# Performance work log

Hardware: AMD Instinct MI355X
Metric: run time of the kernel (lower is better)

Reference implementation:

```python
import math
import jax, jax.numpy as jnp
import numpy as np

HIDDEN = 2880
HEAD_DIM = 64
N_HEADS = 64
N_KV = 8
Q_MULT = N_HEADS // N_KV  # 8
QKV_DIM = HEAD_DIM * (N_HEADS + 2 * N_KV)  # 5120
SLIDING_WINDOW = 128
SM_SCALE = 1.0 / math.sqrt(HEAD_DIM)
ROPE_BASE = 150000.0
ROPE_SCALING = 32.0
INIT_CTX = 4096
NTK_ALPHA = 1.0
NTK_BETA = 32.0
EPS = 1e-5
N_TOKENS = 1536


def rope_tables(n):
    # YaRN-style inv_freq mixing (scaling_factor > 1 branch)
    d = HEAD_DIM
    freq = ROPE_BASE ** (jnp.arange(0, d, 2, dtype=jnp.float32) / d)
    concentration = 0.1 * math.log(ROPE_SCALING) + 1.0
    d_half = d / 2
    low = d_half * math.log(INIT_CTX / (NTK_BETA * 2 * math.pi)) / math.log(ROPE_BASE)
    high = d_half * math.log(INIT_CTX / (NTK_ALPHA * 2 * math.pi)) / math.log(ROPE_BASE)
    interpolation = 1.0 / (ROPE_SCALING * freq)
    extrapolation = 1.0 / freq
    ramp = (jnp.arange(d_half, dtype=jnp.float32) - low) / (high - low)
    mask = 1.0 - jnp.clip(ramp, 0.0, 1.0)
    inv_freq = interpolation * (1.0 - mask) + extrapolation * mask
    t = jnp.arange(n, dtype=jnp.float32)
    freqs = t[:, None] * inv_freq[None, :]  # (n, d/2)
    return jnp.cos(freqs) * concentration, jnp.sin(freqs) * concentration


def apply_rotary(x, cos, sin):
    # x: (n, H, d); cos/sin: (n, d/2)
    c = cos[:, None, :]
    s = sin[:, None, :]
    x1, x2 = jnp.split(x, 2, axis=-1)
    return jnp.concatenate([x1 * c - x2 * s, x2 * c + x1 * s], axis=-1)


def setup_inputs() -> dict:
    key = jax.random.key(0)
    ks = jax.random.split(key, 7)
    x = jax.random.normal(ks[0], (N_TOKENS, HIDDEN), dtype=jnp.float32)
    norm_scale = jnp.ones((HIDDEN,), dtype=jnp.float32)
    qkv_w = jax.random.normal(ks[1], (QKV_DIM, HIDDEN), dtype=jnp.float32) * 0.02
    qkv_b = jax.random.normal(ks[2], (QKV_DIM,), dtype=jnp.float32) * 0.02
    out_w = jax.random.normal(ks[3], (HIDDEN, HEAD_DIM * N_HEADS), dtype=jnp.float32) * 0.02
    out_b = jax.random.normal(ks[4], (HIDDEN,), dtype=jnp.float32) * 0.02
    sinks = jax.random.normal(ks[5], (N_HEADS,), dtype=jnp.float32)
    return {"x": x, "norm_scale": norm_scale, "qkv_w": qkv_w, "qkv_b": qkv_b,
            "out_w": out_w, "out_b": out_b, "sinks": sinks}


def reference(x, norm_scale, qkv_w, qkv_b, out_w, out_b, sinks):
    n = x.shape[0]
    # RMSNorm (fp32)
    t = x * jax.lax.rsqrt(jnp.mean(x * x, axis=-1, keepdims=True) + EPS) * norm_scale
    # fused QKV projection
    qkv = t @ qkv_w.T + qkv_b  # (n, QKV_DIM)
    q = qkv[:, : N_HEADS * HEAD_DIM].reshape(n, N_KV, Q_MULT, HEAD_DIM)
    k = qkv[:, N_HEADS * HEAD_DIM : (N_HEADS + N_KV) * HEAD_DIM].reshape(n, N_KV, HEAD_DIM)
    v = qkv[:, (N_HEADS + N_KV) * HEAD_DIM :].reshape(n, N_KV, HEAD_DIM)
    # RoPE
    cos, sin = rope_tables(n)
    q = apply_rotary(q.reshape(n, N_HEADS, HEAD_DIM), cos, sin).reshape(n, N_KV, Q_MULT, HEAD_DIM)
    k = apply_rotary(k, cos, sin)
    # attention with causal + sliding-window mask and sink logits
    i = jnp.arange(n)[:, None]
    j = jnp.arange(n)[None, :]
    allowed = (j <= i) & (j > i - SLIDING_WINDOW)
    mask = jnp.where(allowed, 0.0, -jnp.inf).astype(jnp.float32)  # (q, k)
    scores = jnp.einsum('qhmd,khd->hmqk', q, k) * SM_SCALE + mask[None, None, :, :]
    s = sinks.reshape(N_KV, Q_MULT, 1, 1)
    s = jnp.broadcast_to(s, (N_KV, Q_MULT, n, 1))
    logits = jnp.concatenate([scores, s], axis=-1)
    w = jax.nn.softmax(logits, axis=-1)[..., :-1]  # drop sink column
    attn = jnp.einsum('hmqk,khd->qhmd', w, v).reshape(n, N_HEADS * HEAD_DIM)
    # output projection + residual
    return x + attn @ out_w.T + out_b
```

## Files before the change

### kernel.cpp

```cpp
#include <hip/hip_runtime.h>

typedef __attribute__((ext_vector_type(8))) short bf16x8;
typedef __attribute__((ext_vector_type(4))) float f32x4;

#define HIDDEN 2880
#define QKV_DIM 5120
#define NH 64
#define NKV 8
#define HD 64
#define ATT_DIM 4096
#define WINDOW 128
#define SM_SCALE 0.125f

__device__ __forceinline__ ushort f2bf(float f) {
  union { float f; unsigned u; } a; a.f = f;
  unsigned r = a.u + 0x7fffu + ((a.u >> 16) & 1u);
  return (ushort)(r >> 16);
}
__device__ __forceinline__ float bf2f(ushort u) {
  union { unsigned u; float f; } a; a.u = ((unsigned)u) << 16;
  return a.f;
}

__device__ __forceinline__ void gload_lds16(const void* g, void* l) {
  __builtin_amdgcn_global_load_lds((const __attribute__((address_space(1))) void*)g,
                                   (__attribute__((address_space(3))) void*)l, 16, 0, 0);
}

__global__ __launch_bounds__(256) void cvt_f32_bf16(const float* __restrict__ in,
                                                    ushort* __restrict__ out, int n4) {
  int i = blockIdx.x * blockDim.x + threadIdx.x;
  int stride = gridDim.x * blockDim.x;
  for (; i < n4; i += stride) {
    float4 v = ((const float4*)in)[i];
    ushort4 o = { f2bf(v.x), f2bf(v.y), f2bf(v.z), f2bf(v.w) };
    ((ushort4*)out)[i] = o;
  }
}

__global__ __launch_bounds__(256) void rmsnorm_bf16(const float* __restrict__ x,
                                                    const float* __restrict__ scale,
                                                    ushort* __restrict__ t) {
  int row = blockIdx.x;
  int tid = threadIdx.x;
  const float4* xr = (const float4*)(x + (size_t)row * HIDDEN);
  float4 a0 = xr[tid];
  float4 a1 = xr[tid + 256];
  bool has2 = tid < 208;
  float4 a2 = has2 ? xr[tid + 512] : float4{0.f, 0.f, 0.f, 0.f};
  float ss = a0.x*a0.x + a0.y*a0.y + a0.z*a0.z + a0.w*a0.w
           + a1.x*a1.x + a1.y*a1.y + a1.z*a1.z + a1.w*a1.w
           + a2.x*a2.x + a2.y*a2.y + a2.z*a2.z + a2.w*a2.w;
  for (int m = 1; m < 64; m <<= 1) ss += __shfl_xor(ss, m, 64);
  __shared__ float red[4];
  if ((tid & 63) == 0) red[tid >> 6] = ss;
  __syncthreads();
  ss = red[0] + red[1] + red[2] + red[3];
  float r = rsqrtf(ss / (float)HIDDEN + 1e-5f);
  ushort4* tr = (ushort4*)(t + (size_t)row * HIDDEN);
  const float4* sc4 = (const float4*)scale;
  {
    float4 s = sc4[tid];
    ushort4 o = { f2bf(a0.x*r*s.x), f2bf(a0.y*r*s.y), f2bf(a0.z*r*s.z), f2bf(a0.w*r*s.w) };
    tr[tid] = o;
  }
  {
    float4 s = sc4[tid + 256];
    ushort4 o = { f2bf(a1.x*r*s.x), f2bf(a1.y*r*s.y), f2bf(a1.z*r*s.z), f2bf(a1.w*r*s.w) };
    tr[tid + 256] = o;
  }
  if (has2) {
    float4 s = sc4[tid + 512];
    ushort4 o = { f2bf(a2.x*r*s.x), f2bf(a2.y*r*s.y), f2bf(a2.z*r*s.z), f2bf(a2.w*r*s.w) };
    tr[tid + 512] = o;
  }
}

template <int MASK_N>
__global__ __launch_bounds__(512)
void gemm_8p(const ushort* __restrict__ A, const ushort* __restrict__ B,
             ushort* __restrict__ P, int M, int N, int K, int NSK) {
  __shared__ __align__(16) ushort Al[2][256 * 64];
  __shared__ __align__(16) ushort Bl[2][256 * 64];
  const int tid = threadIdx.x;
  const int wave = tid >> 6, lane = tid & 63;
  const int l15 = lane & 15, hi = lane >> 4;

  int nwg = gridDim.x, orig = blockIdx.x;
  int q8 = nwg >> 3, r8 = nwg & 7, xcd = orig & 7, seq = orig >> 3;
  int swz = (xcd < r8 ? xcd * (q8 + 1) : r8 * (q8 + 1) + (xcd - r8) * q8) + seq;
  int nm = M >> 8;
  int bm = swz % nm, bn = swz / nm;
  const int row0 = bm * 256, col0 = bn * 256;
  const int sk = blockIdx.y;
  const int NTtot = K >> 6;
  const int tt0 = sk * NTtot / NSK, tt1 = (sk + 1) * NTtot / NSK;
  ushort* Pp = P + (size_t)sk * M * N;

  const int wrow = (wave >> 2) * 128;
  const int wcol = (wave & 3) * 64;
  const int srow = lane >> 3;
  const int schunk = (lane & 7) ^ srow;

  f32x4 acc[8][4] = {};

  auto stageA = [&](int t, int r) {
    int row = row0 + r * 64 + wave * 8 + srow;
    gload_lds16(A + (size_t)row * K + (t << 6) + schunk * 8,
                &Al[t & 1][(r * 64 + wave * 8) * 64]);
  };
  auto stageB = [&](int t, int r) {
    int brow = col0 + r * 64 + wave * 8 + srow;
    if (MASK_N) { if (brow > N - 1) brow = N - 1; }
    gload_lds16(B + (size_t)brow * K + (t << 6) + schunk * 8,
                &Bl[t & 1][(r * 64 + wave * 8) * 64]);
  };
  auto stageAll = [&](int t) {
#pragma unroll
    for (int r = 0; r < 4; ++r) { stageA(t, r); stageB(t, r); }
  };
  auto LDA = [&](bf16x8 (&dst)[4][2], int mh, const char* base) {
#pragma unroll
    for (int mt = 0; mt < 4; ++mt)
#pragma unroll
      for (int ks = 0; ks < 2; ++ks) {
        int rr = wrow + mh * 64 + mt * 16 + l15;
        int off = (rr * 128 + ks * 64 + hi * 16) ^ ((rr & 7) << 4);
        dst[mt][ks] = *(const bf16x8*)(base + off);
      }
  };
  auto LDB = [&](bf16x8 (&dst)[2][2], int nh, const char* base) {
#pragma unroll
    for (int nt = 0; nt < 2; ++nt)
#pragma unroll
      for (int ks = 0; ks < 2; ++ks) {
        int rr = wcol + nh * 32 + nt * 16 + l15;
        int off = (rr * 128 + ks * 64 + hi * 16) ^ ((rr & 7) << 4);
        dst[nt][ks] = *(const bf16x8*)(base + off);
      }
  };
  auto MMA = [&](bf16x8 (&a)[4][2], bf16x8 (&b)[2][2], int mh, int nh) {
    __builtin_amdgcn_s_setprio(1);
#pragma unroll
    for (int ks = 0; ks < 2; ++ks)
#pragma unroll
      for (int nt = 0; nt < 2; ++nt)
#pragma unroll
        for (int mt = 0; mt < 4; ++mt)
          acc[mh * 4 + mt][nh * 2 + nt] = __builtin_amdgcn_mfma_f32_16x16x32_bf16(
              a[mt][ks], b[nt][ks], acc[mh * 4 + mt][nh * 2 + nt], 0, 0, 0);
    __builtin_amdgcn_s_setprio(0);
  };

  stageAll(tt0);
  bool two = (tt1 - tt0 > 1);
  if (two) {
    stageAll(tt0 + 1);
    asm volatile("s_waitcnt vmcnt(8)" ::: "memory");
  } else {
    asm volatile("s_waitcnt vmcnt(0)" ::: "memory");
  }
  __builtin_amdgcn_s_barrier();

  for (int t = tt0; t < tt1; ++t) {
    const char* Ab = (const char*)&Al[t & 1][0];
    const char* Bb = (const char*)&Bl[t & 1][0];
    bool pre = (t + 2 < tt1);
    bf16x8 afr[4][2], bf0[2][2], bf1[2][2];
    LDA(afr, 0, Ab);
    LDB(bf0, 0, Bb);
    __builtin_amdgcn_s_barrier();
    MMA(afr, bf0, 0, 0);
    __builtin_amdgcn_s_barrier();
    LDB(bf1, 1, Bb);
    if (pre) { stageA(t + 2, 0); stageA(t + 2, 2); }
    __builtin_amdgcn_s_barrier();
    MMA(afr, bf1, 0, 1);
    __builtin_amdgcn_s_barrier();
    LDA(afr, 1, Ab);
    if (pre) { stageB(t + 2, 0); stageB(t + 2, 1); stageB(t + 2, 2); stageB(t + 2, 3); }
    __builtin_amdgcn_s_barrier();
    MMA(afr, bf1, 1, 1);
    __builtin_amdgcn_s_barrier();
    if (pre) { stageA(t + 2, 1); stageA(t + 2, 3); }
    __builtin_amdgcn_s_barrier();
    MMA(afr, bf0, 1, 0);
    if (pre) asm volatile("s_waitcnt vmcnt(8)" ::: "memory");
    else     asm volatile("s_waitcnt vmcnt(0)" ::: "memory");
    __builtin_amdgcn_s_barrier();
  }

#pragma unroll
  for (int mtg = 0; mtg < 8; ++mtg) {
#pragma unroll
    for (int nt = 0; nt < 4; ++nt) {
#pragma unroll
      for (int rr = 0; rr < 4; ++rr) {
        int row = row0 + wrow + mtg * 16 + (hi << 2) + rr;
        int col = col0 + wcol + nt * 16 + l15;
        if (!MASK_N || col < N) Pp[(size_t)row * N + col] = f2bf(acc[mtg][nt][rr]);
      }
    }
  }
}

__global__ __launch_bounds__(256)
void reduce_out(const float* __restrict__ x, const float* __restrict__ b,
                const ushort* __restrict__ p, int nsk, size_t stride,
                float* __restrict__ out, int n4, int N) {
  int i = blockIdx.x * blockDim.x + threadIdx.x;
  if (i >= n4) return;
  float4 v = ((const float4*)x)[i];
  int col = (i * 4) % N;
  float4 bb = *(const float4*)(b + col);
  v.x += bb.x; v.y += bb.y; v.z += bb.z; v.w += bb.w;
  for (int s = 0; s < nsk; ++s) {
    ushort4 pv = *(const ushort4*)(p + s * stride + (size_t)i * 4);
    v.x += bf2f(pv.x); v.y += bf2f(pv.y); v.z += bf2f(pv.z); v.w += bf2f(pv.w);
  }
  ((float4*)out)[i] = v;
}

__global__ __launch_bounds__(256)
void rope_split(const ushort* __restrict__ p, size_t stride, const float* __restrict__ qkvb,
                ushort* __restrict__ qb, ushort* __restrict__ kb, ushort* __restrict__ vb) {
  int tok = blockIdx.x;
  int tid = threadIdx.x;
  __shared__ float cs[32], sn[32];
  if (tid < 32) {
    float d = (float)tid;
    float freq = powf(150000.0f, d / 32.0f);
    float conc = 0.1f * logf(32.0f) + 1.0f;
    float lg = logf(150000.0f);
    float low = 32.0f * logf(4096.0f / (32.0f * 6.2831853f)) / lg;
    float high = 32.0f * logf(4096.0f / 6.2831853f) / lg;
    float ramp = (d - low) / (high - low);
    float cl = fminf(fmaxf(ramp, 0.0f), 1.0f);
    float mask = 1.0f - cl;
    float inv_freq = (1.0f - mask) / (32.0f * freq) + mask / freq;
    float fr = (float)tok * inv_freq;
    cs[tid] = cosf(fr) * conc;
    sn[tid] = sinf(fr) * conc;
  }
  __syncthreads();
  const ushort* r0 = p + (size_t)tok * QKV_DIM;
  const ushort* r1 = r0 + stride;
  auto ld = [&](int c) { return bf2f(r0[c]) + bf2f(r1[c]) + qkvb[c]; };
#pragma unroll
  for (int it = 0; it < 8; ++it) {
    int pp = tid + it * 256;
    int hd = pp >> 5, d = pp & 31;
    float x1 = ld(hd * 64 + d), x2 = ld(hd * 64 + d + 32);
    float c = cs[d], s = sn[d];
    size_t o = ((size_t)tok * NH + hd) * HD + d;
    qb[o] = f2bf(x1 * c - x2 * s);
    qb[o + 32] = f2bf(x2 * c + x1 * s);
  }
  {
    int pp = tid;
    int hd = pp >> 5, d = pp & 31;
    float x1 = ld(4096 + hd * 64 + d), x2 = ld(4096 + hd * 64 + d + 32);
    float c = cs[d], s = sn[d];
    size_t o = ((size_t)tok * NKV + hd) * HD + d;
    kb[o] = f2bf(x1 * c - x2 * s);
    kb[o + 32] = f2bf(x2 * c + x1 * s);
  }
#pragma unroll
  for (int it = 0; it < 2; ++it) {
    int pp = tid + it * 256;
    vb[(size_t)tok * (NKV * HD) + pp] = f2bf(ld(4608 + pp));
  }
}

__global__ __launch_bounds__(512)
void attn_cvt(const ushort* __restrict__ qb, const ushort* __restrict__ kb,
              const ushort* __restrict__ vb, const float* __restrict__ sinks,
              ushort* __restrict__ attn, int n, int nattn,
              const float* __restrict__ w, ushort* __restrict__ wout, int n4w) {
  __shared__ __align__(16) ushort Kl[160 * 64];
  __shared__ __align__(16) ushort Vt[64 * 168];
  __shared__ __align__(16) ushort Pl[8][16 * 40];
  int tid = threadIdx.x;
  if ((int)blockIdx.x >= nattn) {
    int i = ((int)blockIdx.x - nattn) * 512 + tid;
    int stride = (gridDim.x - nattn) * 512;
    for (; i < n4w; i += stride) {
      float4 v = ((const float4*)w)[i];
      ushort4 o = { f2bf(v.x), f2bf(v.y), f2bf(v.z), f2bf(v.w) };
      ((ushort4*)wout)[i] = o;
    }
    return;
  }
  int wave = tid >> 6, lane = tid & 63;
  int l15 = lane & 15, hi = lane >> 4;
  int qstart = ((int)blockIdx.x >> 3) * 16;
  int kv = (int)blockIdx.x & 7;
  int head = kv * 8 + wave;
  int key0 = qstart - 128;

  for (int i = 0; i < 3; ++i) {
    int rowb = i * 64 + wave * 8;
    if (rowb < 160) {
      int r = rowb + (lane >> 3);
      int gj = key0 + r; if (gj < 0) gj = 0;
      int chunk = (lane & 7) ^ (lane >> 3);
      gload_lds16(kb + ((size_t)gj * NKV + kv) * HD + chunk * 8, Kl + rowb * 64);
    }
  }
  for (int e = tid; e < 160 * 16; e += 512) {
    int j = e >> 4, d4 = (e & 15) << 2;
    int gj = key0 + j; if (gj < 0) gj = 0;
    ushort4 v = *(const ushort4*)(vb + ((size_t)gj * NKV + kv) * HD + d4);
    Vt[(d4 + 0) * 168 + j] = v.x;
    Vt[(d4 + 1) * 168 + j] = v.y;
    Vt[(d4 + 2) * 168 + j] = v.z;
    Vt[(d4 + 3) * 168 + j] = v.w;
  }
  bf16x8 qf[2];
#pragma unroll
  for (int ks = 0; ks < 2; ++ks) {
    int r = qstart + l15;
    int kk = ks * 32 + hi * 8;
    qf[ks] = *(const bf16x8*)(qb + ((size_t)r * NH + head) * HD + kk);
  }
  __syncthreads();

  f32x4 s[10] = {};
#pragma unroll
  for (int nt = 0; nt < 10; ++nt) {
#pragma unroll
    for (int ks = 0; ks < 2; ++ks) {
      int r = nt * 16 + l15;
      int off = (r * 128 + (ks * 32 + hi * 8) * 2) ^ ((r & 7) << 4);
      bf16x8 kf = *(const bf16x8*)((const char*)Kl + off);
      s[nt] = __builtin_amdgcn_mfma_f32_16x16x32_bf16(qf[ks], kf, s[nt], 0, 0, 0);
    }
  }

  float lrow[4];
  float snk = sinks[head];
#pragma unroll
  for (int r = 0; r < 4; ++r) {
    int i = qstart + hi * 4 + r;
    float mx = -1e30f;
#pragma unroll
    for (int nt = 0; nt < 10; ++nt) {
      int j = key0 + nt * 16 + l15;
      bool ok = (j >= 0) && (j <= i) && (j > i - WINDOW);
      float val = ok ? s[nt][r] * SM_SCALE : -1e30f;
      s[nt][r] = val;
      mx = fmaxf(mx, val);
    }
    mx = fmaxf(mx, __shfl_xor(mx, 1, 64));
    mx = fmaxf(mx, __shfl_xor(mx, 2, 64));
    mx = fmaxf(mx, __shfl_xor(mx, 4, 64));
    mx = fmaxf(mx, __shfl_xor(mx, 8, 64));
    mx = fmaxf(mx, snk);
    float sum = 0.f;
#pragma unroll
    for (int nt = 0; nt < 10; ++nt) {
      float pv = __expf(s[nt][r] - mx);
      s[nt][r] = pv;
      sum += pv;
    }
    sum += __shfl_xor(sum, 1, 64);
    sum += __shfl_xor(sum, 2, 64);
    sum += __shfl_xor(sum, 4, 64);
    sum += __shfl_xor(sum, 8, 64);
    sum += __expf(snk - mx);
    lrow[r] = sum;
  }

  f32x4 o[4] = {};
#pragma unroll
  for (int kc = 0; kc < 5; ++kc) {
#pragma unroll
    for (int t2 = 0; t2 < 2; ++t2) {
      int nt = kc * 2 + t2;
#pragma unroll
      for (int r = 0; r < 4; ++r)
        Pl[wave][(hi * 4 + r) * 40 + t2 * 16 + l15] = f2bf(s[nt][r]);
    }
    bf16x8 pa = *(const bf16x8*)(&Pl[wave][l15 * 40 + hi * 8]);
#pragma unroll
    for (int nt = 0; nt < 4; ++nt) {
      int d = nt * 16 + l15;
      int kk = kc * 32 + hi * 8;
      bf16x8 vf = *(const bf16x8*)(&Vt[d * 168 + kk]);
      o[nt] = __builtin_amdgcn_mfma_f32_16x16x32_bf16(pa, vf, o[nt], 0, 0, 0);
    }
  }

#pragma unroll
  for (int nt = 0; nt < 4; ++nt)
#pragma unroll
    for (int r = 0; r < 4; ++r) {
      int row = qstart + hi * 4 + r;
      int d = nt * 16 + l15;
      float val = o[nt][r] / lrow[r];
      attn[((size_t)row * NH + head) * HD + d] = f2bf(val);
    }
}

extern "C" void kernel_launch(void* const* d_in, const int* in_sizes, int n_in,
                              void* d_out, int out_size, void* d_ws, size_t ws_size,
                              hipStream_t stream) {
  const float* x      = (const float*)d_in[0];
  const float* nscale = (const float*)d_in[1];
  const float* qkv_w  = (const float*)d_in[2];
  const float* qkv_b  = (const float*)d_in[3];
  const float* out_w  = (const float*)d_in[4];
  const float* out_b  = (const float*)d_in[5];
  const float* sinks  = (const float*)d_in[6];
  float* out = (float*)d_out;
  int n = in_sizes[0] / HIDDEN;

  char* ws = (char*)d_ws;
  size_t off = 0;
  auto alloc = [&](size_t bytes) {
    char* p = ws + off;
    off += (bytes + 255) & ~(size_t)255;
    return p;
  };
  ushort* t_bf    = (ushort*)alloc((size_t)n * HIDDEN * 2);
  ushort* qkvw_bf = (ushort*)alloc((size_t)QKV_DIM * HIDDEN * 2);
  ushort* outw_bf = (ushort*)alloc((size_t)HIDDEN * ATT_DIM * 2);
  ushort* q_bf    = (ushort*)alloc((size_t)n * NH * HD * 2);
  ushort* k_bf    = (ushort*)alloc((size_t)n * NKV * HD * 2);
  ushort* v_bf    = (ushort*)alloc((size_t)n * NKV * HD * 2);
  ushort* attn    = (ushort*)alloc((size_t)n * ATT_DIM * 2);
  size_t qkv_ps = (size_t)n * QKV_DIM;
  size_t out_ps = (size_t)n * HIDDEN;
  size_t pelems = 2 * qkv_ps > 3 * out_ps ? 2 * qkv_ps : 3 * out_ps;
  ushort* partials = (ushort*)alloc(pelems * 2);

  cvt_f32_bf16<<<1024, 256, 0, stream>>>(qkv_w, qkvw_bf, QKV_DIM * HIDDEN / 4);
  rmsnorm_bf16<<<n, 256, 0, stream>>>(x, nscale, t_bf);
  gemm_8p<0><<<dim3((n / 256) * (QKV_DIM / 256), 2), 512, 0, stream>>>(
      t_bf, qkvw_bf, partials, n, QKV_DIM, HIDDEN, 2);
  rope_split<<<n, 256, 0, stream>>>(partials, qkv_ps, qkv_b, q_bf, k_bf, v_bf);
  int nattn = (n / 16) * NKV;
  attn_cvt<<<nattn + 320, 512, 0, stream>>>(q_bf, k_bf, v_bf, sinks, attn, n, nattn,
                                            out_w, outw_bf, HIDDEN * ATT_DIM / 4);
  gemm_8p<1><<<dim3((n / 256) * 12, 3), 512, 0, stream>>>(
      attn, outw_bf, partials, n, HIDDEN, ATT_DIM, 3);
  reduce_out<<<(n * HIDDEN / 4 + 255) / 256, 256, 0, stream>>>(
      x, out_b, partials, 3, out_ps, out, n * HIDDEN / 4, HIDDEN);
}
```

Before: 168.6 us.

## Shrink GEMM tiles to 128x128, drop QKV split-K, fuse bias and norm/convert kernels

```diff
diff --git a/kernel.cpp b/kernel.cpp
--- a/kernel.cpp
+++ b/kernel.cpp
@@ -27,22 +27,22 @@
                                    (__attribute__((address_space(3))) void*)l, 16, 0, 0);
 }
 
-__global__ __launch_bounds__(256) void cvt_f32_bf16(const float* __restrict__ in,
-                                                    ushort* __restrict__ out, int n4) {
-  int i = blockIdx.x * blockDim.x + threadIdx.x;
-  int stride = gridDim.x * blockDim.x;
-  for (; i < n4; i += stride) {
-    float4 v = ((const float4*)in)[i];
-    ushort4 o = { f2bf(v.x), f2bf(v.y), f2bf(v.z), f2bf(v.w) };
-    ((ushort4*)out)[i] = o;
-  }
-}
-
-__global__ __launch_bounds__(256) void rmsnorm_bf16(const float* __restrict__ x,
-                                                    const float* __restrict__ scale,
-                                                    ushort* __restrict__ t) {
+__global__ __launch_bounds__(256)
+void norm_cvt(const float* __restrict__ x, const float* __restrict__ scale,
+              ushort* __restrict__ t, int n,
+              const float* __restrict__ w, ushort* __restrict__ wout, int n4w) {
+  int tid = threadIdx.x;
+  if ((int)blockIdx.x >= n) {
+    int i = ((int)blockIdx.x - n) * 256 + tid;
+    int stride = (gridDim.x - n) * 256;
+    for (; i < n4w; i += stride) {
+      float4 v = ((const float4*)w)[i];
+      ushort4 o = { f2bf(v.x), f2bf(v.y), f2bf(v.z), f2bf(v.w) };
+      ((ushort4*)wout)[i] = o;
+    }
+    return;
+  }
   int row = blockIdx.x;
-  int tid = threadIdx.x;
   const float4* xr = (const float4*)(x + (size_t)row * HIDDEN);
   float4 a0 = xr[tid];
   float4 a1 = xr[tid + 256];
@@ -76,12 +76,13 @@
   }
 }
 
-template <int MASK_N>
-__global__ __launch_bounds__(512)
-void gemm_8p(const ushort* __restrict__ A, const ushort* __restrict__ B,
-             ushort* __restrict__ P, int M, int N, int K, int NSK) {
-  __shared__ __align__(16) ushort Al[2][256 * 64];
-  __shared__ __align__(16) ushort Bl[2][256 * 64];
+template <int MASK_N, int FUSE_BIAS>
+__global__ __launch_bounds__(256)
+void gemm_128(const ushort* __restrict__ A, const ushort* __restrict__ B,
+              const float* __restrict__ bias, ushort* __restrict__ P,
+              int M, int N, int K, int NSK) {
+  __shared__ __align__(16) ushort Al[2][128 * 64];
+  __shared__ __align__(16) ushort Bl[2][128 * 64];
   const int tid = threadIdx.x;
   const int wave = tid >> 6, lane = tid & 63;
   const int l15 = lane & 15, hi = lane >> 4;
@@ -89,42 +90,43 @@
   int nwg = gridDim.x, orig = blockIdx.x;
   int q8 = nwg >> 3, r8 = nwg & 7, xcd = orig & 7, seq = orig >> 3;
   int swz = (xcd < r8 ? xcd * (q8 + 1) : r8 * (q8 + 1) + (xcd - r8) * q8) + seq;
-  int nm = M >> 8;
+  int nm = M >> 7;
   int bm = swz % nm, bn = swz / nm;
-  const int row0 = bm * 256, col0 = bn * 256;
+  const int row0 = bm * 128, col0 = bn * 128;
   const int sk = blockIdx.y;
   const int NTtot = K >> 6;
   const int tt0 = sk * NTtot / NSK, tt1 = (sk + 1) * NTtot / NSK;
   ushort* Pp = P + (size_t)sk * M * N;
 
-  const int wrow = (wave >> 2) * 128;
-  const int wcol = (wave & 3) * 64;
+  const int wrow = (wave >> 1) * 64;
+  const int wcol = (wave & 1) * 64;
   const int srow = lane >> 3;
   const int schunk = (lane & 7) ^ srow;
 
-  f32x4 acc[8][4] = {};
+  f32x4 acc[4][4] = {};
 
   auto stageA = [&](int t, int r) {
-    int row = row0 + r * 64 + wave * 8 + srow;
-    gload_lds16(A + (size_t)row * K + (t << 6) + schunk * 8,
-                &Al[t & 1][(r * 64 + wave * 8) * 64]);
+    int rowb = r * 32 + wave * 8;
+    gload_lds16(A + (size_t)(row0 + rowb + srow) * K + (t << 6) + schunk * 8,
+                &Al[t & 1][rowb * 64]);
   };
   auto stageB = [&](int t, int r) {
-    int brow = col0 + r * 64 + wave * 8 + srow;
+    int rowb = r * 32 + wave * 8;
+    int brow = col0 + rowb + srow;
     if (MASK_N) { if (brow > N - 1) brow = N - 1; }
     gload_lds16(B + (size_t)brow * K + (t << 6) + schunk * 8,
-                &Bl[t & 1][(r * 64 + wave * 8) * 64]);
+                &Bl[t & 1][rowb * 64]);
   };
   auto stageAll = [&](int t) {
 #pragma unroll
     for (int r = 0; r < 4; ++r) { stageA(t, r); stageB(t, r); }
   };
-  auto LDA = [&](bf16x8 (&dst)[4][2], int mh, const char* base) {
-#pragma unroll
-    for (int mt = 0; mt < 4; ++mt)
+  auto LDA = [&](bf16x8 (&dst)[2][2], int mh, const char* base) {
+#pragma unroll
+    for (int mt = 0; mt < 2; ++mt)
 #pragma unroll
       for (int ks = 0; ks < 2; ++ks) {
-        int rr = wrow + mh * 64 + mt * 16 + l15;
+        int rr = wrow + (mh * 2 + mt) * 16 + l15;
         int off = (rr * 128 + ks * 64 + hi * 16) ^ ((rr & 7) << 4);
         dst[mt][ks] = *(const bf16x8*)(base + off);
       }
@@ -134,21 +136,21 @@
     for (int nt = 0; nt < 2; ++nt)
 #pragma unroll
       for (int ks = 0; ks < 2; ++ks) {
-        int rr = wcol + nh * 32 + nt * 16 + l15;
+        int rr = wcol + (nh * 2 + nt) * 16 + l15;
         int off = (rr * 128 + ks * 64 + hi * 16) ^ ((rr & 7) << 4);
         dst[nt][ks] = *(const bf16x8*)(base + off);
       }
   };
-  auto MMA = [&](bf16x8 (&a)[4][2], bf16x8 (&b)[2][2], int mh, int nh) {
+  auto MMA = [&](bf16x8 (&a)[2][2], bf16x8 (&b)[2][2], int mh, int nh) {
     __builtin_amdgcn_s_setprio(1);
 #pragma unroll
     for (int ks = 0; ks < 2; ++ks)
 #pragma unroll
       for (int nt = 0; nt < 2; ++nt)
 #pragma unroll
-        for (int mt = 0; mt < 4; ++mt)
-          acc[mh * 4 + mt][nh * 2 + nt] = __builtin_amdgcn_mfma_f32_16x16x32_bf16(
-              a[mt][ks], b[nt][ks], acc[mh * 4 + mt][nh * 2 + nt], 0, 0, 0);
+        for (int mt = 0; mt < 2; ++mt)
+          acc[mh * 2 + mt][nh * 2 + nt] = __builtin_amdgcn_mfma_f32_16x16x32_bf16(
+              a[mt][ks], b[nt][ks], acc[mh * 2 + mt][nh * 2 + nt], 0, 0, 0);
     __builtin_amdgcn_s_setprio(0);
   };
 
@@ -166,7 +168,7 @@
     const char* Ab = (const char*)&Al[t & 1][0];
     const char* Bb = (const char*)&Bl[t & 1][0];
     bool pre = (t + 2 < tt1);
-    bf16x8 afr[4][2], bf0[2][2], bf1[2][2];
+    bf16x8 afr[2][2], bf0[2][2], bf1[2][2];
     LDA(afr, 0, Ab);
     LDB(bf0, 0, Bb);
     __builtin_amdgcn_s_barrier();
@@ -191,14 +193,18 @@
   }
 
 #pragma unroll
-  for (int mtg = 0; mtg < 8; ++mtg) {
+  for (int mt = 0; mt < 4; ++mt) {
 #pragma unroll
     for (int nt = 0; nt < 4; ++nt) {
 #pragma unroll
       for (int rr = 0; rr < 4; ++rr) {
-        int row = row0 + wrow + mtg * 16 + (hi << 2) + rr;
+        int row = row0 + wrow + mt * 16 + (hi << 2) + rr;
         int col = col0 + wcol + nt * 16 + l15;
-        if (!MASK_N || col < N) Pp[(size_t)row * N + col] = f2bf(acc[mtg][nt][rr]);
+        if (!MASK_N || col < N) {
+          float v = acc[mt][nt][rr];
+          if (FUSE_BIAS) v += bias[col];
+          Pp[(size_t)row * N + col] = f2bf(v);
+        }
       }
     }
   }
@@ -222,7 +228,7 @@
 }
 
 __global__ __launch_bounds__(256)
-void rope_split(const ushort* __restrict__ p, size_t stride, const float* __restrict__ qkvb,
+void rope_split(const ushort* __restrict__ qkv,
                 ushort* __restrict__ qb, ushort* __restrict__ kb, ushort* __restrict__ vb) {
   int tok = blockIdx.x;
   int tid = threadIdx.x;
@@ -243,14 +249,12 @@
     sn[tid] = sinf(fr) * conc;
   }
   __syncthreads();
-  const ushort* r0 = p + (size_t)tok * QKV_DIM;
-  const ushort* r1 = r0 + stride;
-  auto ld = [&](int c) { return bf2f(r0[c]) + bf2f(r1[c]) + qkvb[c]; };
+  const ushort* row = qkv + (size_t)tok * QKV_DIM;
 #pragma unroll
   for (int it = 0; it < 8; ++it) {
     int pp = tid + it * 256;
     int hd = pp >> 5, d = pp & 31;
-    float x1 = ld(hd * 64 + d), x2 = ld(hd * 64 + d + 32);
+    float x1 = bf2f(row[hd * 64 + d]), x2 = bf2f(row[hd * 64 + d + 32]);
     float c = cs[d], s = sn[d];
     size_t o = ((size_t)tok * NH + hd) * HD + d;
     qb[o] = f2bf(x1 * c - x2 * s);
@@ -259,7 +263,7 @@
   {
     int pp = tid;
     int hd = pp >> 5, d = pp & 31;
-    float x1 = ld(4096 + hd * 64 + d), x2 = ld(4096 + hd * 64 + d + 32);
+    float x1 = bf2f(row[4096 + hd * 64 + d]), x2 = bf2f(row[4096 + hd * 64 + d + 32]);
     float c = cs[d], s = sn[d];
     size_t o = ((size_t)tok * NKV + hd) * HD + d;
     kb[o] = f2bf(x1 * c - x2 * s);
@@ -268,7 +272,7 @@
 #pragma unroll
   for (int it = 0; it < 2; ++it) {
     int pp = tid + it * 256;
-    vb[(size_t)tok * (NKV * HD) + pp] = f2bf(ld(4608 + pp));
+    vb[(size_t)tok * (NKV * HD) + pp] = row[4608 + pp];
   }
 }
 
@@ -425,25 +429,24 @@
   ushort* t_bf    = (ushort*)alloc((size_t)n * HIDDEN * 2);
   ushort* qkvw_bf = (ushort*)alloc((size_t)QKV_DIM * HIDDEN * 2);
   ushort* outw_bf = (ushort*)alloc((size_t)HIDDEN * ATT_DIM * 2);
+  ushort* qkv_bf  = (ushort*)alloc((size_t)n * QKV_DIM * 2);
   ushort* q_bf    = (ushort*)alloc((size_t)n * NH * HD * 2);
   ushort* k_bf    = (ushort*)alloc((size_t)n * NKV * HD * 2);
   ushort* v_bf    = (ushort*)alloc((size_t)n * NKV * HD * 2);
   ushort* attn    = (ushort*)alloc((size_t)n * ATT_DIM * 2);
-  size_t qkv_ps = (size_t)n * QKV_DIM;
   size_t out_ps = (size_t)n * HIDDEN;
-  size_t pelems = 2 * qkv_ps > 3 * out_ps ? 2 * qkv_ps : 3 * out_ps;
-  ushort* partials = (ushort*)alloc(pelems * 2);
-
-  cvt_f32_bf16<<<1024, 256, 0, stream>>>(qkv_w, qkvw_bf, QKV_DIM * HIDDEN / 4);
-  rmsnorm_bf16<<<n, 256, 0, stream>>>(x, nscale, t_bf);
-  gemm_8p<0><<<dim3((n / 256) * (QKV_DIM / 256), 2), 512, 0, stream>>>(
-      t_bf, qkvw_bf, partials, n, QKV_DIM, HIDDEN, 2);
-  rope_split<<<n, 256, 0, stream>>>(partials, qkv_ps, qkv_b, q_bf, k_bf, v_bf);
+  ushort* partials = (ushort*)alloc(2 * out_ps * 2);
+
+  norm_cvt<<<n + 1024, 256, 0, stream>>>(x, nscale, t_bf, n,
+                                         qkv_w, qkvw_bf, QKV_DIM * HIDDEN / 4);
+  gemm_128<0, 1><<<dim3((n / 128) * (QKV_DIM / 128), 1), 256, 0, stream>>>(
+      t_bf, qkvw_bf, qkv_b, qkv_bf, n, QKV_DIM, HIDDEN, 1);
+  rope_split<<<n, 256, 0, stream>>>(qkv_bf, q_bf, k_bf, v_bf);
   int nattn = (n / 16) * NKV;
   attn_cvt<<<nattn + 320, 512, 0, stream>>>(q_bf, k_bf, v_bf, sinks, attn, n, nattn,
                                             out_w, outw_bf, HIDDEN * ATT_DIM / 4);
-  gemm_8p<1><<<dim3((n / 256) * 12, 3), 512, 0, stream>>>(
-      attn, outw_bf, partials, n, HIDDEN, ATT_DIM, 3);
+  gemm_128<1, 0><<<dim3((n / 128) * 23, 2), 256, 0, stream>>>(
+      attn, outw_bf, nullptr, partials, n, HIDDEN, ATT_DIM, 2);
   reduce_out<<<(n * HIDDEN / 4 + 255) / 256, 256, 0, stream>>>(
-      x, out_b, partials, 3, out_ps, out, n * HIDDEN / 4, HIDDEN);
-}
+      x, out_b, partials, 2, out_ps, out, n * HIDDEN / 4, HIDDEN);
+}
```

Result: slower. 203.0 us (+20.4%).

## Use 256x192 tiles for output GEMM and fuse rmsnorm with weight conversion

Applied to the files above, without the earlier changes.

```diff
diff --git a/kernel.cpp b/kernel.cpp
--- a/kernel.cpp
+++ b/kernel.cpp
@@ -27,22 +27,22 @@
                                    (__attribute__((address_space(3))) void*)l, 16, 0, 0);
 }
 
-__global__ __launch_bounds__(256) void cvt_f32_bf16(const float* __restrict__ in,
-                                                    ushort* __restrict__ out, int n4) {
-  int i = blockIdx.x * blockDim.x + threadIdx.x;
-  int stride = gridDim.x * blockDim.x;
-  for (; i < n4; i += stride) {
-    float4 v = ((const float4*)in)[i];
-    ushort4 o = { f2bf(v.x), f2bf(v.y), f2bf(v.z), f2bf(v.w) };
-    ((ushort4*)out)[i] = o;
-  }
-}
-
-__global__ __launch_bounds__(256) void rmsnorm_bf16(const float* __restrict__ x,
-                                                    const float* __restrict__ scale,
-                                                    ushort* __restrict__ t) {
+__global__ __launch_bounds__(256)
+void norm_cvt(const float* __restrict__ x, const float* __restrict__ scale,
+              ushort* __restrict__ t, int n,
+              const float* __restrict__ w, ushort* __restrict__ wout, int n4w) {
+  int tid = threadIdx.x;
+  if ((int)blockIdx.x >= n) {
+    int i = ((int)blockIdx.x - n) * 256 + tid;
+    int stride = (gridDim.x - n) * 256;
+    for (; i < n4w; i += stride) {
+      float4 v = ((const float4*)w)[i];
+      ushort4 o = { f2bf(v.x), f2bf(v.y), f2bf(v.z), f2bf(v.w) };
+      ((ushort4*)wout)[i] = o;
+    }
+    return;
+  }
   int row = blockIdx.x;
-  int tid = threadIdx.x;
   const float4* xr = (const float4*)(x + (size_t)row * HIDDEN);
   float4 a0 = xr[tid];
   float4 a1 = xr[tid + 256];
@@ -76,12 +76,13 @@
   }
 }
 
-template <int MASK_N>
+template <int NFRAG>
 __global__ __launch_bounds__(512)
 void gemm_8p(const ushort* __restrict__ A, const ushort* __restrict__ B,
              ushort* __restrict__ P, int M, int N, int K, int NSK) {
+  constexpr int N1 = NFRAG - 2;
   __shared__ __align__(16) ushort Al[2][256 * 64];
-  __shared__ __align__(16) ushort Bl[2][256 * 64];
+  __shared__ __align__(16) ushort Bl[2][NFRAG * 64 * 64];
   const int tid = threadIdx.x;
   const int wave = tid >> 6, lane = tid & 63;
   const int l15 = lane & 15, hi = lane >> 4;
@@ -91,18 +92,18 @@
   int swz = (xcd < r8 ? xcd * (q8 + 1) : r8 * (q8 + 1) + (xcd - r8) * q8) + seq;
   int nm = M >> 8;
   int bm = swz % nm, bn = swz / nm;
-  const int row0 = bm * 256, col0 = bn * 256;
+  const int row0 = bm * 256, col0 = bn * (64 * NFRAG);
   const int sk = blockIdx.y;
   const int NTtot = K >> 6;
   const int tt0 = sk * NTtot / NSK, tt1 = (sk + 1) * NTtot / NSK;
   ushort* Pp = P + (size_t)sk * M * N;
 
   const int wrow = (wave >> 2) * 128;
-  const int wcol = (wave & 3) * 64;
+  const int wcol = (wave & 3) * (16 * NFRAG);
   const int srow = lane >> 3;
   const int schunk = (lane & 7) ^ srow;
 
-  f32x4 acc[8][4] = {};
+  f32x4 acc[8][NFRAG] = {};
 
   auto stageA = [&](int t, int r) {
     int row = row0 + r * 64 + wave * 8 + srow;
@@ -111,13 +112,14 @@
   };
   auto stageB = [&](int t, int r) {
     int brow = col0 + r * 64 + wave * 8 + srow;
-    if (MASK_N) { if (brow > N - 1) brow = N - 1; }
     gload_lds16(B + (size_t)brow * K + (t << 6) + schunk * 8,
                 &Bl[t & 1][(r * 64 + wave * 8) * 64]);
   };
   auto stageAll = [&](int t) {
 #pragma unroll
-    for (int r = 0; r < 4; ++r) { stageA(t, r); stageB(t, r); }
+    for (int r = 0; r < 4; ++r) stageA(t, r);
+#pragma unroll
+    for (int r = 0; r < NFRAG; ++r) stageB(t, r);
   };
   auto LDA = [&](bf16x8 (&dst)[4][2], int mh, const char* base) {
 #pragma unroll
@@ -129,17 +131,27 @@
         dst[mt][ks] = *(const bf16x8*)(base + off);
       }
   };
-  auto LDB = [&](bf16x8 (&dst)[2][2], int nh, const char* base) {
+  auto LDB_lo = [&](bf16x8 (&dst)[2][2], const char* base) {
 #pragma unroll
     for (int nt = 0; nt < 2; ++nt)
 #pragma unroll
       for (int ks = 0; ks < 2; ++ks) {
-        int rr = wcol + nh * 32 + nt * 16 + l15;
+        int rr = wcol + nt * 16 + l15;
         int off = (rr * 128 + ks * 64 + hi * 16) ^ ((rr & 7) << 4);
         dst[nt][ks] = *(const bf16x8*)(base + off);
       }
   };
-  auto MMA = [&](bf16x8 (&a)[4][2], bf16x8 (&b)[2][2], int mh, int nh) {
+  auto LDB_hi = [&](bf16x8 (&dst)[2][2], const char* base) {
+#pragma unroll
+    for (int nt = 0; nt < N1; ++nt)
+#pragma unroll
+      for (int ks = 0; ks < 2; ++ks) {
+        int rr = wcol + (2 + nt) * 16 + l15;
+        int off = (rr * 128 + ks * 64 + hi * 16) ^ ((rr & 7) << 4);
+        dst[nt][ks] = *(const bf16x8*)(base + off);
+      }
+  };
+  auto MMA_lo = [&](bf16x8 (&a)[4][2], bf16x8 (&b)[2][2], int mh) {
     __builtin_amdgcn_s_setprio(1);
 #pragma unroll
     for (int ks = 0; ks < 2; ++ks)
@@ -147,8 +159,20 @@
       for (int nt = 0; nt < 2; ++nt)
 #pragma unroll
         for (int mt = 0; mt < 4; ++mt)
-          acc[mh * 4 + mt][nh * 2 + nt] = __builtin_amdgcn_mfma_f32_16x16x32_bf16(
-              a[mt][ks], b[nt][ks], acc[mh * 4 + mt][nh * 2 + nt], 0, 0, 0);
+          acc[mh * 4 + mt][nt] = __builtin_amdgcn_mfma_f32_16x16x32_bf16(
+              a[mt][ks], b[nt][ks], acc[mh * 4 + mt][nt], 0, 0, 0);
+    __builtin_amdgcn_s_setprio(0);
+  };
+  auto MMA_hi = [&](bf16x8 (&a)[4][2], bf16x8 (&b)[2][2], int mh) {
+    __builtin_amdgcn_s_setprio(1);
+#pragma unroll
+    for (int ks = 0; ks < 2; ++ks)
+#pragma unroll
+      for (int nt = 0; nt < N1; ++nt)
+#pragma unroll
+        for (int mt = 0; mt < 4; ++mt)
+          acc[mh * 4 + mt][2 + nt] = __builtin_amdgcn_mfma_f32_16x16x32_bf16(
+              a[mt][ks], b[nt][ks], acc[mh * 4 + mt][2 + nt], 0, 0, 0);
     __builtin_amdgcn_s_setprio(0);
   };
 
@@ -156,7 +180,8 @@
   bool two = (tt1 - tt0 > 1);
   if (two) {
     stageAll(tt0 + 1);
-    asm volatile("s_waitcnt vmcnt(8)" ::: "memory");
+    if constexpr (NFRAG == 4) asm volatile("s_waitcnt vmcnt(8)" ::: "memory");
+    else                      asm volatile("s_waitcnt vmcnt(7)" ::: "memory");
   } else {
     asm volatile("s_waitcnt vmcnt(0)" ::: "memory");
   }
@@ -168,37 +193,44 @@
     bool pre = (t + 2 < tt1);
     bf16x8 afr[4][2], bf0[2][2], bf1[2][2];
     LDA(afr, 0, Ab);
-    LDB(bf0, 0, Bb);
-    __builtin_amdgcn_s_barrier();
-    MMA(afr, bf0, 0, 0);
-    __builtin_amdgcn_s_barrier();
-    LDB(bf1, 1, Bb);
+    LDB_lo(bf0, Bb);
+    __builtin_amdgcn_s_barrier();
+    MMA_lo(afr, bf0, 0);
+    __builtin_amdgcn_s_barrier();
+    LDB_hi(bf1, Bb);
     if (pre) { stageA(t + 2, 0); stageA(t + 2, 2); }
     __builtin_amdgcn_s_barrier();
-    MMA(afr, bf1, 0, 1);
+    MMA_hi(afr, bf1, 0);
     __builtin_amdgcn_s_barrier();
     LDA(afr, 1, Ab);
-    if (pre) { stageB(t + 2, 0); stageB(t + 2, 1); stageB(t + 2, 2); stageB(t + 2, 3); }
-    __builtin_amdgcn_s_barrier();
-    MMA(afr, bf1, 1, 1);
+    if (pre) {
+#pragma unroll
+      for (int r = 0; r < NFRAG; ++r) stageB(t + 2, r);
+    }
+    __builtin_amdgcn_s_barrier();
+    MMA_hi(afr, bf1, 1);
     __builtin_amdgcn_s_barrier();
     if (pre) { stageA(t + 2, 1); stageA(t + 2, 3); }
     __builtin_amdgcn_s_barrier();
-    MMA(afr, bf0, 1, 0);
-    if (pre) asm volatile("s_waitcnt vmcnt(8)" ::: "memory");
-    else     asm volatile("s_waitcnt vmcnt(0)" ::: "memory");
+    MMA_lo(afr, bf0, 1);
+    if (pre) {
+      if constexpr (NFRAG == 4) asm volatile("s_waitcnt vmcnt(8)" ::: "memory");
+      else                      asm volatile("s_waitcnt vmcnt(7)" ::: "memory");
+    } else {
+      asm volatile("s_waitcnt vmcnt(0)" ::: "memory");
+    }
     __builtin_amdgcn_s_barrier();
   }
 
 #pragma unroll
   for (int mtg = 0; mtg < 8; ++mtg) {
 #pragma unroll
-    for (int nt = 0; nt < 4; ++nt) {
+    for (int nt = 0; nt < NFRAG; ++nt) {
 #pragma unroll
       for (int rr = 0; rr < 4; ++rr) {
         int row = row0 + wrow + mtg * 16 + (hi << 2) + rr;
         int col = col0 + wcol + nt * 16 + l15;
-        if (!MASK_N || col < N) Pp[(size_t)row * N + col] = f2bf(acc[mtg][nt][rr]);
+        Pp[(size_t)row * N + col] = f2bf(acc[mtg][nt][rr]);
       }
     }
   }
@@ -434,15 +466,15 @@
   size_t pelems = 2 * qkv_ps > 3 * out_ps ? 2 * qkv_ps : 3 * out_ps;
   ushort* partials = (ushort*)alloc(pelems * 2);
 
-  cvt_f32_bf16<<<1024, 256, 0, stream>>>(qkv_w, qkvw_bf, QKV_DIM * HIDDEN / 4);
-  rmsnorm_bf16<<<n, 256, 0, stream>>>(x, nscale, t_bf);
-  gemm_8p<0><<<dim3((n / 256) * (QKV_DIM / 256), 2), 512, 0, stream>>>(
+  norm_cvt<<<n + 1024, 256, 0, stream>>>(x, nscale, t_bf, n,
+                                         qkv_w, qkvw_bf, QKV_DIM * HIDDEN / 4);
+  gemm_8p<4><<<dim3((n / 256) * (QKV_DIM / 256), 2), 512, 0, stream>>>(
       t_bf, qkvw_bf, partials, n, QKV_DIM, HIDDEN, 2);
   rope_split<<<n, 256, 0, stream>>>(partials, qkv_ps, qkv_b, q_bf, k_bf, v_bf);
   int nattn = (n / 16) * NKV;
   attn_cvt<<<nattn + 320, 512, 0, stream>>>(q_bf, k_bf, v_bf, sinks, attn, n, nattn,
                                             out_w, outw_bf, HIDDEN * ATT_DIM / 4);
-  gemm_8p<1><<<dim3((n / 256) * 12, 3), 512, 0, stream>>>(
+  gemm_8p<3><<<dim3((n / 256) * (HIDDEN / 192), 3), 512, 0, stream>>>(
       attn, outw_bf, partials, n, HIDDEN, ATT_DIM, 3);
   reduce_out<<<(n * HIDDEN / 4 + 255) / 256, 256, 0, stream>>>(
       x, out_b, partials, 3, out_ps, out, n * HIDDEN / 4, HIDDEN);
```

Result: slower. 194.8 us (+15.5%).
